# Kernel tuning notes

Hardware: AMD Instinct MI355X
Metric: run time of the kernel (lower is better)

Reference implementation:

```python
import jax, jax.numpy as jnp
import numpy as np


def setup_inputs() -> dict:
    key = jax.random.key(0)
    k1, k2, k3 = jax.random.split(key, 3)
    B, E, S = 8, 2048, 2048
    x = jax.random.normal(k1, (B, E, S), dtype=jnp.float32)
    weight = jax.random.normal(k2, (1, S), dtype=jnp.float32)
    diag_weight = jax.random.normal(k3, (1, S), dtype=jnp.float32)
    bias = jnp.zeros((S,), dtype=jnp.float32)
    decay_value = jnp.ones((2, 1), dtype=jnp.float32)
    return {"x": x, "weight": weight, "diag_weight": diag_weight,
            "bias": bias, "decay_value": decay_value}


def _build_matrix(weight, diag_weight, decay_value):
    # Upper-triangular (strict) decay matrix M[i,j] = v[i] * d**(j-i) for j>i,
    # plus diagonal M[j,j] = v2[j].  d = clip(decay_value[1], 0.9, 1.0).
    v = weight.reshape(-1)       # (S,)
    v2 = diag_weight.reshape(-1)  # (S,)
    S = v.shape[0]
    idx = jnp.arange(S)
    diff = idx[None, :] - idx[:, None]          # j - i, shape (S, S)
    d = jnp.clip(decay_value[1, 0], 0.9, 1.0)   # scalar
    strict_upper = jnp.where(diff > 0, v[:, None] * d ** diff, jnp.zeros((), dtype=v.dtype))
    return strict_upper + jnp.diag(v2)          # (S, S)


def reference(x, weight, diag_weight, bias, decay_value):
    # x: (B, E, S); mixes along the sequence axis with the causal-decay matrix.
    M = _build_matrix(weight, diag_weight, decay_value)
    out = jnp.einsum('bes,st->bet', x, M) + bias  # bias broadcasts over last (seq) dim
    return out
```

## Files before the change

kernel.cpp:

```cpp
#include <hip/hip_runtime.h>


#define SEQ 2048
#define THREADS 512
#define PER_THREAD 4

__global__ __launch_bounds__(THREADS) void decay_scan_kernel(
    const float* __restrict__ x,
    const float* __restrict__ weight,
    const float* __restrict__ diag_weight,
    const float* __restrict__ bias,
    const float* __restrict__ decay,
    float* __restrict__ out)
{
    const int tid  = threadIdx.x;
    const int lane = tid & 63;
    const int wv   = tid >> 6;
    const long base = (long)blockIdx.x * SEQ;
    const int off  = tid * PER_THREAD;

    float d = fminf(fmaxf(decay[1], 0.9f), 1.0f);
    const float d2 = d * d, d3 = d2 * d, d4 = d2 * d2;

    const float4 xv = *(const float4*)(x + base + off);
    const float4 vv = *(const float4*)(weight + off);
    const float4 gv = *(const float4*)(diag_weight + off);
    const float4 bv = *(const float4*)(bias + off);

    const float xa[4] = {xv.x, xv.y, xv.z, xv.w};
    const float va[4] = {vv.x, vv.y, vv.z, vv.w};

    float lp[PER_THREAD];
    float c = 0.f;
    #pragma unroll
    for (int k = 0; k < PER_THREAD; ++k) {
        lp[k] = c;
        c = d * fmaf(xa[k], va[k], c);
    }

    float s = c, p = d4;
    #pragma unroll
    for (int o = 1; o < 64; o <<= 1) {
        const float s2 = __shfl_up(s, o, 64);
        const float p2 = __shfl_up(p, o, 64);
        if (lane >= o) { s = fmaf(s2, p, s); p = p2 * p; }
    }
    float es = __shfl_up(s, 1, 64);
    float ep = __shfl_up(p, 1, 64);
    if (lane == 0) { es = 0.f; ep = 1.f; }

    __shared__ float ws[8], wp[8];
    if (lane == 63) { ws[wv] = s; wp[wv] = p; }
    __syncthreads();
    float cs = 0.f;
    #pragma unroll
    for (int w = 0; w < 7; ++w) {
        if (w < wv) cs = fmaf(cs, wp[w], ws[w]);
    }
    const float C = fmaf(cs, ep, es);

    float4 o4;
    o4.x = fmaf(xa[0], gv.x, C            + lp[0] + bv.x);
    o4.y = fmaf(xa[1], gv.y, fmaf(C, d,  lp[1]) + bv.y);
    o4.z = fmaf(xa[2], gv.z, fmaf(C, d2, lp[2]) + bv.z);
    o4.w = fmaf(xa[3], gv.w, fmaf(C, d3, lp[3]) + bv.w);
    *(float4*)(out + base + off) = o4;
}

extern "C" void kernel_launch(void* const* d_in, const int* in_sizes, int n_in,
                              void* d_out, int out_size, void* d_ws, size_t ws_size,
                              hipStream_t stream) {
    const float* x           = (const float*)d_in[0];
    const float* weight      = (const float*)d_in[1];
    const float* diag_weight = (const float*)d_in[2];
    const float* bias        = (const float*)d_in[3];
    const float* decay       = (const float*)d_in[4];
    float* out = (float*)d_out;

    const int rows = in_sizes[0] / SEQ;
    decay_scan_kernel<<<rows, THREADS, 0, stream>>>(
        x, weight, diag_weight, bias, decay, out);
}
```

Baseline: 237.8 us.

## Process multiple rows per block with precomputed decay powers and prefetch

```diff
diff --git a/kernel.cpp b/kernel.cpp
--- a/kernel.cpp
+++ b/kernel.cpp
@@ -3,9 +3,9 @@
 
 #define SEQ 2048
 #define THREADS 512
-#define PER_THREAD 4
+#define ROWS_PER_BLOCK 8
 
-__global__ __launch_bounds__(THREADS) void decay_scan_kernel(
+__global__ __launch_bounds__(THREADS, 8) void decay_scan_kernel(
     const float* __restrict__ x,
     const float* __restrict__ weight,
     const float* __restrict__ diag_weight,
@@ -16,55 +16,73 @@
     const int tid  = threadIdx.x;
     const int lane = tid & 63;
     const int wv   = tid >> 6;
-    const long base = (long)blockIdx.x * SEQ;
-    const int off  = tid * PER_THREAD;
+    const int off  = tid * 4;
+    const long base = (long)blockIdx.x * ROWS_PER_BLOCK * SEQ;
 
-    float d = fminf(fmaxf(decay[1], 0.9f), 1.0f);
-    const float d2 = d * d, d3 = d2 * d, d4 = d2 * d2;
+    const float d = fminf(fmaxf(decay[1], 0.9f), 1.0f);
+    const float d2 = d * d, d3 = d2 * d;
 
-    const float4 xv = *(const float4*)(x + base + off);
+    float dq[7];
+    dq[0] = d2 * d2;
+    #pragma unroll
+    for (int k = 1; k < 7; ++k) dq[k] = dq[k - 1] * dq[k - 1];
+    const float d256 = dq[6];
+    float dpow = 1.f;
+    #pragma unroll
+    for (int k = 0; k < 6; ++k) if ((lane >> k) & 1) dpow *= dq[k];
+
     const float4 vv = *(const float4*)(weight + off);
     const float4 gv = *(const float4*)(diag_weight + off);
     const float4 bv = *(const float4*)(bias + off);
 
-    const float xa[4] = {xv.x, xv.y, xv.z, xv.w};
-    const float va[4] = {vv.x, vv.y, vv.z, vv.w};
+    __shared__ float ws[2][8];
 
-    float lp[PER_THREAD];
-    float c = 0.f;
+    float4 xv = *(const float4*)(x + base + off);
+
     #pragma unroll
-    for (int k = 0; k < PER_THREAD; ++k) {
-        lp[k] = c;
-        c = d * fmaf(xa[k], va[k], c);
+    for (int r = 0; r < ROWS_PER_BLOCK; ++r) {
+        float4 xn;
+        if (r + 1 < ROWS_PER_BLOCK)
+            xn = *(const float4*)(x + base + (long)(r + 1) * SEQ + off);
+
+        const float xa[4] = {xv.x, xv.y, xv.z, xv.w};
+
+        float lp1, lp2, lp3;
+        float c;
+        c = d * (xa[0] * vv.x);            lp1 = c;
+        c = d * fmaf(xa[1], vv.y, c);      lp2 = c;
+        c = d * fmaf(xa[2], vv.z, c);      lp3 = c;
+        c = d * fmaf(xa[3], vv.w, c);
+
+        float s = c;
+        #pragma unroll
+        for (int k = 0; k < 6; ++k) {
+            const int o = 1 << k;
+            const float s2 = __shfl_up(s, o, 64);
+            if (lane >= o) s = fmaf(s2, dq[k], s);
+        }
+        float es = __shfl_up(s, 1, 64);
+        if (lane == 0) es = 0.f;
+
+        if (lane == 63) ws[r & 1][wv] = s;
+        __syncthreads();
+        float cs = 0.f;
+        const float* wrow = ws[r & 1];
+        #pragma unroll
+        for (int w = 0; w < 7; ++w) {
+            if (w < wv) cs = fmaf(cs, d256, wrow[w]);
+        }
+        const float C = fmaf(cs, dpow, es);
+
+        float4 o4;
+        o4.x = fmaf(xa[0], gv.x, C                + bv.x);
+        o4.y = fmaf(xa[1], gv.y, fmaf(C, d,  lp1) + bv.y);
+        o4.z = fmaf(xa[2], gv.z, fmaf(C, d2, lp2) + bv.z);
+        o4.w = fmaf(xa[3], gv.w, fmaf(C, d3, lp3) + bv.w);
+        *(float4*)(out + base + (long)r * SEQ + off) = o4;
+
+        xv = xn;
     }
-
-    float s = c, p = d4;
-    #pragma unroll
-    for (int o = 1; o < 64; o <<= 1) {
-        const float s2 = __shfl_up(s, o, 64);
-        const float p2 = __shfl_up(p, o, 64);
-        if (lane >= o) { s = fmaf(s2, p, s); p = p2 * p; }
-    }
-    float es = __shfl_up(s, 1, 64);
-    float ep = __shfl_up(p, 1, 64);
-    if (lane == 0) { es = 0.f; ep = 1.f; }
-
-    __shared__ float ws[8], wp[8];
-    if (lane == 63) { ws[wv] = s; wp[wv] = p; }
-    __syncthreads();
-    float cs = 0.f;
-    #pragma unroll
-    for (int w = 0; w < 7; ++w) {
-        if (w < wv) cs = fmaf(cs, wp[w], ws[w]);
-    }
-    const float C = fmaf(cs, ep, es);
-
-    float4 o4;
-    o4.x = fmaf(xa[0], gv.x, C            + lp[0] + bv.x);
-    o4.y = fmaf(xa[1], gv.y, fmaf(C, d,  lp[1]) + bv.y);
-    o4.z = fmaf(xa[2], gv.z, fmaf(C, d2, lp[2]) + bv.z);
-    o4.w = fmaf(xa[3], gv.w, fmaf(C, d3, lp[3]) + bv.w);
-    *(float4*)(out + base + off) = o4;
 }
 
 extern "C" void kernel_launch(void* const* d_in, const int* in_sizes, int n_in,
@@ -78,6 +96,6 @@
     float* out = (float*)d_out;
 
     const int rows = in_sizes[0] / SEQ;
-    decay_scan_kernel<<<rows, THREADS, 0, stream>>>(
+    decay_scan_kernel<<<rows / ROWS_PER_BLOCK, THREADS, 0, stream>>>(
         x, weight, diag_weight, bias, decay, out);
 }
```

Result: no change. 242.1 us (+1.8%).
